# Performance work log

Measured on AMD Instinct MI355X. Metric: run time of the kernel, lower is better.

The kernel has to match this reference:

```python
import jax, jax.numpy as jnp
import numpy as np

N_X_POINTS = 100
IN_FEATURES = 2
OUT_FEATURES = 512
BATCH = 8192


def make_grid():
    # torch.meshgrid default indexing='ij'; stack flattened, transpose -> [K, in_features]
    axes = [jnp.linspace(0.0, 1.0, N_X_POINTS, dtype=jnp.float32) for _ in range(IN_FEATURES)]
    mesh = jnp.meshgrid(*axes, indexing='ij')
    return jnp.stack([m.ravel() for m in mesh]).T  # [10000, 2]


def setup_inputs() -> dict:
    key = jax.random.key(0)
    k1, k2, k3, k4 = jax.random.split(key, 4)
    X = jax.random.normal(k1, (BATCH, OUT_FEATURES), dtype=jnp.float32)
    # nn.Linear(in_features=2, out_features=512): weight [512, 2], bias [512]
    W = jax.random.normal(k2, (OUT_FEATURES, IN_FEATURES), dtype=jnp.float32) * (1.0 / np.sqrt(IN_FEATURES))
    b = jax.random.normal(k3, (OUT_FEATURES,), dtype=jnp.float32) * 0.1
    betta = jax.random.uniform(k4, (1,), dtype=jnp.float32)  # torch.rand(1)
    grid = make_grid()
    return {"X": X, "W": W, "b": b, "betta": betta, "grid": grid}


def reference(X, W, b, betta, grid):
    # GTMEstimator.transform with method='mean', mean=0, std=1.
    yg = grid @ W.T + b                                   # y(grid): [K, D]
    # squared euclidean distances: cdist(yg, X)^2 -> [K, N]
    d2 = (jnp.sum(yg * yg, axis=1)[:, None]
          + jnp.sum(X * X, axis=1)[None, :]
          - 2.0 * (yg @ X.T))
    logits = (-betta[0] / 2.0) * d2                       # [K, N]
    # p = (betta/2pi)^(D/2) * exp(logits); p_x = p / p.sum(axis=0).
    # The constant cancels in normalization, so this is exactly softmax over the grid axis
    # (numerically stable form of the original computation).
    p_x = jax.nn.softmax(logits, axis=0)                  # [K, N]
    return p_x.T @ grid                                   # (grid.T @ p_x).T -> [N, in_features]
```

## Files before the change

kernel.cpp:

```cpp
#include <hip/hip_runtime.h>
#include <math.h>

#ifndef __has_builtin
#define __has_builtin(x) 0
#endif
#if __has_builtin(__builtin_amdgcn_exp2f)
#define EXP2F(x) __builtin_amdgcn_exp2f(x)
#else
#define EXP2F(x) exp2f(x)
#endif

typedef float v2f __attribute__((ext_vector_type(2)));

namespace {

constexpr int DIM    = 512;
constexpr int NBATCH = 8192;
constexpr int WPB    = 4;
constexpr int SPW    = 2;
constexpr int BLOCK  = WPB * 64;
constexpr float INV99 = 1.0f / 99.0f;
constexpr float LOG2E = 1.4426950408889634f;

__global__ __launch_bounds__(BLOCK) void gtm_final_kernel(
    const float* __restrict__ X, const float* __restrict__ W,
    const float* __restrict__ b, const float* __restrict__ betta,
    float* __restrict__ out) {
  __shared__ float sTab[WPB][100][4];
  __shared__ float sEC[WPB][128][SPW];

  const int lane = threadIdx.x & 63;
  const int wave = threadIdx.x >> 6;
  const int n0 = blockIdx.x * (WPB * SPW) + wave * SPW;

  float4 xr[SPW][2];
  #pragma unroll
  for (int s = 0; s < SPW; ++s) {
    const float4* Xv = reinterpret_cast<const float4*>(X + (size_t)(n0 + s) * DIM);
    xr[s][0] = Xv[lane * 2];
    xr[s][1] = Xv[lane * 2 + 1];
  }
  float w0[8], w1[8], bb[8];
  {
    const float4* Wv = reinterpret_cast<const float4*>(W);
    #pragma unroll
    for (int j = 0; j < 4; ++j) {
      float4 wv = Wv[lane * 4 + j];
      w0[2*j]   = wv.x; w1[2*j]   = wv.y;
      w0[2*j+1] = wv.z; w1[2*j+1] = wv.w;
    }
    const float4* bv = reinterpret_cast<const float4*>(b);
    float4 ba = bv[lane*2], bc = bv[lane*2+1];
    bb[0]=ba.x; bb[1]=ba.y; bb[2]=ba.z; bb[3]=ba.w;
    bb[4]=bc.x; bb[5]=bc.y; bb[6]=bc.z; bb[7]=bc.w;
  }

  float q11=0.f, q12=0.f, q22=0.f, u0=0.f, u1=0.f;
  #pragma unroll
  for (int j = 0; j < 8; ++j) {
    q11 = fmaf(w0[j], w0[j], q11); q12 = fmaf(w0[j], w1[j], q12);
    q22 = fmaf(w1[j], w1[j], q22);
    u0  = fmaf(w0[j], bb[j], u0);  u1  = fmaf(w1[j], bb[j], u1);
  }
  float pa[SPW], pc[SPW];
  #pragma unroll
  for (int s = 0; s < SPW; ++s) {
    float xx[8] = {xr[s][0].x, xr[s][0].y, xr[s][0].z, xr[s][0].w,
                   xr[s][1].x, xr[s][1].y, xr[s][1].z, xr[s][1].w};
    float a = 0.f, c = 0.f;
    #pragma unroll
    for (int j = 0; j < 8; ++j) {
      a = fmaf(w0[j], xx[j], a);
      c = fmaf(w1[j], xx[j], c);
    }
    pa[s] = a; pc[s] = c;
  }
  #pragma unroll
  for (int off = 32; off; off >>= 1) {
    q11 += __shfl_xor(q11, off, 64); q12 += __shfl_xor(q12, off, 64);
    q22 += __shfl_xor(q22, off, 64);
    u0  += __shfl_xor(u0,  off, 64); u1  += __shfl_xor(u1,  off, 64);
    #pragma unroll
    for (int s = 0; s < SPW; ++s) {
      pa[s] += __shfl_xor(pa[s], off, 64);
      pc[s] += __shfl_xor(pc[s], off, 64);
    }
  }

  const float lam = betta[0] * LOG2E;
  const float cX  = -lam * q12;
  const float aF  = -0.5f * lam * q11, aG = -0.5f * lam * q22;
  const float gi1 = lane * INV99, gi2 = (lane + 64) * INV99;
  const bool hiOk = (lane + 64) < 100;

  const float rcpF = -1.f / (2.f * aF);
  const float rcpG = -1.f / (2.f * aG);
  float mF[SPW], mG[SPW], bFv[SPW], bGv[SPW];
  #pragma unroll
  for (int s = 0; s < SPW; ++s) {
    const float bF = lam * (pa[s] - u0), bG = lam * (pc[s] - u1);
    bFv[s] = bF; bGv[s] = bG;
    float gf = fminf(fmaxf(bF * rcpF, 0.f), 1.f);
    float gg = fminf(fmaxf(bG * rcpG, 0.f), 1.f);
    mF[s] = gf * fmaf(aF, gf, bF);
    mG[s] = gg * fmaf(aG, gg, bG);
  }

  const float gaF1 = aF * gi1 * gi1, gaF2 = aF * gi2 * gi2;
  const float gaG1 = aG * gi1 * gi1, gaG2 = aG * gi2 * gi2;
  {
    float er0 = EXP2F(fmaf(gi1, bFv[0], gaF1) - mF[0]);
    float er1 = EXP2F(fmaf(gi1, bFv[1], gaF1) - mF[1]);
    *reinterpret_cast<float4*>(&sTab[wave][lane][0]) =
        make_float4(er0, er1, gi1 * er0, gi1 * er1);
    sEC[wave][lane][0] = EXP2F(fmaf(gi1, bGv[0], gaG1) - mG[0]);
    sEC[wave][lane][1] = EXP2F(fmaf(gi1, bGv[1], gaG1) - mG[1]);
    if (hiOk) {
      float e20 = EXP2F(fmaf(gi2, bFv[0], gaF2) - mF[0]);
      float e21 = EXP2F(fmaf(gi2, bFv[1], gaF2) - mF[1]);
      *reinterpret_cast<float4*>(&sTab[wave][lane + 64][0]) =
          make_float4(e20, e21, gi2 * e20, gi2 * e21);
      sEC[wave][lane + 64][0] = EXP2F(fmaf(gi2, bGv[0], gaG2) - mG[0]);
      sEC[wave][lane + 64][1] = EXP2F(fmaf(gi2, bGv[1], gaG2) - mG[1]);
    } else {
      sEC[wave][lane + 64][0] = 0.f;
      sEC[wave][lane + 64][1] = 0.f;
    }
  }

  const float r1 = EXP2F(cX * gi1 * INV99);
  const float r2 = EXP2F(cX * gi2 * INV99);
  float R1 = r1 * r1; R1 *= R1;
  float R2 = r2 * r2; R2 *= R2;
  float pw1 = 1.f, pw2 = 1.f;

  v2f T1[4], U1[4], T2[4], U2[4];
  #pragma unroll
  for (int m = 0; m < 4; ++m) {
    T1[m]=(v2f)0.f; U1[m]=(v2f)0.f; T2[m]=(v2f)0.f; U2[m]=(v2f)0.f;
  }

  const float4* tab = reinterpret_cast<const float4*>(&sTab[wave][0][0]);
  for (int c = 0; c < 25; ++c) {
    float4 t[4];
    t[0] = tab[4*c];     t[1] = tab[4*c + 1];
    t[2] = tab[4*c + 2]; t[3] = tab[4*c + 3];
    #pragma unroll
    for (int m = 0; m < 4; ++m) {
      const v2f er  = {t[m].x, t[m].y};
      const v2f erg = {t[m].z, t[m].w};
      T1[m] += er  * pw1;
      U1[m] += erg * pw1;
      T2[m] += er  * pw2;
      U2[m] += erg * pw2;
    }
    pw1 *= R1; pw2 *= R2;
  }

  const float r1b = r1 * r1, r1c = r1b * r1;
  const float r2b = r2 * r2, r2c = r2b * r2;
  v2f Tc1 = T1[0] + r1*T1[1] + r1b*T1[2] + r1c*T1[3];
  v2f Uc1 = U1[0] + r1*U1[1] + r1b*U1[2] + r1c*U1[3];
  v2f Tc2 = T2[0] + r2*T2[1] + r2b*T2[2] + r2c*T2[3];
  v2f Uc2 = U2[0] + r2*U2[1] + r2b*U2[2] + r2c*U2[3];

  const v2f ec1v = {sEC[wave][lane][0],      sEC[wave][lane][1]};
  const v2f ec2v = {sEC[wave][lane + 64][0], sEC[wave][lane + 64][1]};
  const v2f ct1 = ec1v * Tc1, ct2 = ec2v * Tc2;
  v2f S   = ct1 + ct2;
  v2f Sg0 = ec1v * Uc1 + ec2v * Uc2;
  v2f Sg1 = ct1 * gi1 + ct2 * gi2;

  #pragma unroll
  for (int off = 32; off; off >>= 1) {
    S.x   += __shfl_xor(S.x,   off, 64); S.y   += __shfl_xor(S.y,   off, 64);
    Sg0.x += __shfl_xor(Sg0.x, off, 64); Sg0.y += __shfl_xor(Sg0.y, off, 64);
    Sg1.x += __shfl_xor(Sg1.x, off, 64); Sg1.y += __shfl_xor(Sg1.y, off, 64);
  }
  if (lane < SPW) {
    const float sv = lane ? S.y   : S.x;
    const float g0 = lane ? Sg0.y : Sg0.x;
    const float g1 = lane ? Sg1.y : Sg1.x;
    const float inv = 1.f / sv;
    reinterpret_cast<float2*>(out)[n0 + lane] = make_float2(g0 * inv, g1 * inv);
  }
}

}

extern "C" void kernel_launch(void* const* d_in, const int* in_sizes, int n_in,
                              void* d_out, int out_size, void* d_ws, size_t ws_size,
                              hipStream_t stream) {
  const float* X     = (const float*)d_in[0];
  const float* W     = (const float*)d_in[1];
  const float* b     = (const float*)d_in[2];
  const float* betta = (const float*)d_in[3];
  float* out = (float*)d_out;
  (void)d_ws; (void)ws_size;

  gtm_final_kernel<<<NBATCH / (WPB * SPW), BLOCK, 0, stream>>>(X, W, b, betta, out);
}
```

Before: 14.85 us.

## Split projection dot products and lattice softmax into two kernels

Result: slower. 17.47 us (+17.6%).

```diff
diff --git a/kernel.cpp b/kernel.cpp
--- a/kernel.cpp
+++ b/kernel.cpp
@@ -22,10 +22,68 @@
 constexpr float INV99 = 1.0f / 99.0f;
 constexpr float LOG2E = 1.4426950408889634f;
 
-__global__ __launch_bounds__(BLOCK) void gtm_final_kernel(
+__global__ __launch_bounds__(256) void dots_kernel(
     const float* __restrict__ X, const float* __restrict__ W,
-    const float* __restrict__ b, const float* __restrict__ betta,
-    float* __restrict__ out) {
+    const float* __restrict__ b, float2* __restrict__ pac,
+    float* __restrict__ qbuf) {
+  const int lane = threadIdx.x & 63;
+  const int wave = threadIdx.x >> 6;
+  const int n = blockIdx.x * 4 + wave;
+
+  float w0[8], w1[8];
+  const float4* Wv = reinterpret_cast<const float4*>(W);
+  #pragma unroll
+  for (int j = 0; j < 4; ++j) {
+    float4 wv = Wv[lane * 4 + j];
+    w0[2*j]   = wv.x; w1[2*j]   = wv.y;
+    w0[2*j+1] = wv.z; w1[2*j+1] = wv.w;
+  }
+
+  const float4* Xv = reinterpret_cast<const float4*>(X + (size_t)n * DIM);
+  float4 xa = Xv[lane*2], xb = Xv[lane*2+1];
+  float xx[8] = {xa.x, xa.y, xa.z, xa.w, xb.x, xb.y, xb.z, xb.w};
+  float pa = 0.f, pc = 0.f;
+  #pragma unroll
+  for (int j = 0; j < 8; ++j) {
+    pa = fmaf(w0[j], xx[j], pa);
+    pc = fmaf(w1[j], xx[j], pc);
+  }
+  #pragma unroll
+  for (int off = 32; off; off >>= 1) {
+    pa += __shfl_xor(pa, off, 64);
+    pc += __shfl_xor(pc, off, 64);
+  }
+  if (lane == 0) pac[n] = make_float2(pa, pc);
+
+  if (blockIdx.x == 0 && wave == 0) {
+    const float4* bv = reinterpret_cast<const float4*>(b);
+    float4 ba = bv[lane*2], bc = bv[lane*2+1];
+    float bb[8] = {ba.x, ba.y, ba.z, ba.w, bc.x, bc.y, bc.z, bc.w};
+    float q11=0.f, q12=0.f, q22=0.f, u0=0.f, u1=0.f;
+    #pragma unroll
+    for (int j = 0; j < 8; ++j) {
+      q11 = fmaf(w0[j], w0[j], q11);
+      q12 = fmaf(w0[j], w1[j], q12);
+      q22 = fmaf(w1[j], w1[j], q22);
+      u0  = fmaf(w0[j], bb[j], u0);
+      u1  = fmaf(w1[j], bb[j], u1);
+    }
+    #pragma unroll
+    for (int off = 32; off; off >>= 1) {
+      q11 += __shfl_xor(q11, off, 64); q12 += __shfl_xor(q12, off, 64);
+      q22 += __shfl_xor(q22, off, 64);
+      u0  += __shfl_xor(u0,  off, 64); u1  += __shfl_xor(u1,  off, 64);
+    }
+    if (lane == 0) {
+      qbuf[0] = q11; qbuf[1] = q12; qbuf[2] = q22;
+      qbuf[3] = u0;  qbuf[4] = u1;
+    }
+  }
+}
+
+__global__ __launch_bounds__(BLOCK) void lattice_kernel(
+    const float2* __restrict__ pac, const float* __restrict__ qbuf,
+    const float* __restrict__ betta, float* __restrict__ out) {
   __shared__ float sTab[WPB][100][4];
   __shared__ float sEC[WPB][128][SPW];
 
@@ -33,59 +91,11 @@
   const int wave = threadIdx.x >> 6;
   const int n0 = blockIdx.x * (WPB * SPW) + wave * SPW;
 
-  float4 xr[SPW][2];
-  #pragma unroll
-  for (int s = 0; s < SPW; ++s) {
-    const float4* Xv = reinterpret_cast<const float4*>(X + (size_t)(n0 + s) * DIM);
-    xr[s][0] = Xv[lane * 2];
-    xr[s][1] = Xv[lane * 2 + 1];
-  }
-  float w0[8], w1[8], bb[8];
-  {
-    const float4* Wv = reinterpret_cast<const float4*>(W);
-    #pragma unroll
-    for (int j = 0; j < 4; ++j) {
-      float4 wv = Wv[lane * 4 + j];
-      w0[2*j]   = wv.x; w1[2*j]   = wv.y;
-      w0[2*j+1] = wv.z; w1[2*j+1] = wv.w;
-    }
-    const float4* bv = reinterpret_cast<const float4*>(b);
-    float4 ba = bv[lane*2], bc = bv[lane*2+1];
-    bb[0]=ba.x; bb[1]=ba.y; bb[2]=ba.z; bb[3]=ba.w;
-    bb[4]=bc.x; bb[5]=bc.y; bb[6]=bc.z; bb[7]=bc.w;
-  }
-
-  float q11=0.f, q12=0.f, q22=0.f, u0=0.f, u1=0.f;
-  #pragma unroll
-  for (int j = 0; j < 8; ++j) {
-    q11 = fmaf(w0[j], w0[j], q11); q12 = fmaf(w0[j], w1[j], q12);
-    q22 = fmaf(w1[j], w1[j], q22);
-    u0  = fmaf(w0[j], bb[j], u0);  u1  = fmaf(w1[j], bb[j], u1);
-  }
-  float pa[SPW], pc[SPW];
-  #pragma unroll
-  for (int s = 0; s < SPW; ++s) {
-    float xx[8] = {xr[s][0].x, xr[s][0].y, xr[s][0].z, xr[s][0].w,
-                   xr[s][1].x, xr[s][1].y, xr[s][1].z, xr[s][1].w};
-    float a = 0.f, c = 0.f;
-    #pragma unroll
-    for (int j = 0; j < 8; ++j) {
-      a = fmaf(w0[j], xx[j], a);
-      c = fmaf(w1[j], xx[j], c);
-    }
-    pa[s] = a; pc[s] = c;
-  }
-  #pragma unroll
-  for (int off = 32; off; off >>= 1) {
-    q11 += __shfl_xor(q11, off, 64); q12 += __shfl_xor(q12, off, 64);
-    q22 += __shfl_xor(q22, off, 64);
-    u0  += __shfl_xor(u0,  off, 64); u1  += __shfl_xor(u1,  off, 64);
-    #pragma unroll
-    for (int s = 0; s < SPW; ++s) {
-      pa[s] += __shfl_xor(pa[s], off, 64);
-      pc[s] += __shfl_xor(pc[s], off, 64);
-    }
-  }
+  const float4 pp = *reinterpret_cast<const float4*>(&pac[n0]);
+  const float q11 = qbuf[0], q12 = qbuf[1], q22 = qbuf[2];
+  const float u0 = qbuf[3], u1 = qbuf[4];
+  const float pa[SPW] = {pp.x, pp.z};
+  const float pc[SPW] = {pp.y, pp.w};
 
   const float lam = betta[0] * LOG2E;
   const float cX  = -lam * q12;
@@ -196,7 +206,11 @@
   const float* b     = (const float*)d_in[2];
   const float* betta = (const float*)d_in[3];
   float* out = (float*)d_out;
-  (void)d_ws; (void)ws_size;
-
-  gtm_final_kernel<<<NBATCH / (WPB * SPW), BLOCK, 0, stream>>>(X, W, b, betta, out);
-}
+
+  float2* pac = (float2*)d_ws;
+  float* qbuf = (float*)d_ws + 2 * NBATCH;
+
+  dots_kernel<<<NBATCH / 4, 256, 0, stream>>>(X, W, b, pac, qbuf);
+
+  lattice_kernel<<<NBATCH / (WPB * SPW), BLOCK, 0, stream>>>(pac, qbuf, betta, out);
+}
```
